# Kernel tuning notes

Measured on AMD Instinct MI355X. Metric: run time of the kernel, lower is better.

Reference implementation:

```python
import jax, jax.numpy as jnp
import numpy as np

N = 50000      # nodes
E = 800000     # edges (avg degree 16)
F_IN = 64      # node_feature_dim
D = 128        # hidden_dim == output_dim
L = 3          # num_gnn_layers
B = 8          # number of graphs in the batch
GATE_H = 128   # GraphAttentionPool hidden_dim default


def _ln(x, g, b, eps=1e-5):
    m = x.mean(-1, keepdims=True)
    v = ((x - m) ** 2).mean(-1, keepdims=True)
    return (x - m) * jax.lax.rsqrt(v + eps) * g + b


def _gelu(x):
    return jax.nn.gelu(x, approximate=False)  # torch F.gelu default = exact erf


def setup_inputs() -> dict:
    key = jax.random.key(0)
    ks = jax.random.split(key, 12)
    p = lambda k, shape: (jax.random.normal(k, shape, jnp.float32) * 0.02)
    return {
        "x": jax.random.normal(ks[0], (N, F_IN), jnp.float32),
        "edge_index": jax.random.randint(ks[1], (2, E), 0, N, dtype=jnp.int32),
        "batch": jnp.sort(jax.random.randint(ks[2], (N,), 0, B, dtype=jnp.int32)),
        # input_proj: Linear + LayerNorm
        "w_in": p(ks[3], (F_IN, D)), "b_in": jnp.zeros((D,), jnp.float32),
        "ln_in_g": jnp.ones((D,), jnp.float32), "ln_in_b": jnp.zeros((D,), jnp.float32),
        # fallback GNN layers (stacked: all layers are 2D -> D)
        "gnn_w": p(ks[4], (L, 2 * D, D)), "gnn_b": jnp.zeros((L, D), jnp.float32),
        "gnn_ln_g": jnp.ones((L, D), jnp.float32), "gnn_ln_b": jnp.zeros((L, D), jnp.float32),
        # outer per-layer norms
        "norm_g": jnp.ones((L, D), jnp.float32), "norm_b": jnp.zeros((L, D), jnp.float32),
        # attention pool gate: Linear(D,128) -> tanh -> Linear(128,1)
        "gate_w1": p(ks[5], (D, GATE_H)), "gate_b1": jnp.zeros((GATE_H,), jnp.float32),
        "gate_w2": p(ks[6], (GATE_H,)), "gate_b2": jnp.zeros((), jnp.float32),
        # out_proj: Linear + LayerNorm + GELU
        "out_w": p(ks[7], (D, D)), "out_b": jnp.zeros((D,), jnp.float32),
        "out_ln_g": jnp.ones((D,), jnp.float32), "out_ln_b": jnp.zeros((D,), jnp.float32),
    }


def reference(x, edge_index, batch, w_in, b_in, ln_in_g, ln_in_b,
              gnn_w, gnn_b, gnn_ln_g, gnn_ln_b, norm_g, norm_b,
              gate_w1, gate_b1, gate_w2, gate_b2,
              out_w, out_b, out_ln_g, out_ln_b):
    src, dst = edge_index[0], edge_index[1]
    n = x.shape[0]

    # input_proj: Linear -> LayerNorm -> GELU
    h = _gelu(_ln(x @ w_in + b_in, ln_in_g, ln_in_b))

    # in-degree count (same every layer), clamped to >= 1
    deg = jax.ops.segment_sum(jnp.ones((src.shape[0],), h.dtype), dst, num_segments=n)
    deg = jnp.maximum(deg, 1.0)[:, None]  # (N, 1)

    for i in range(L):
        # mean-neighbor aggregation: gather x[src], scatter-add to dst
        agg = jax.ops.segment_sum(h[src], dst, num_segments=n) / deg  # (N, D)
        out = jnp.concatenate([h, agg], axis=-1) @ gnn_w[i] + gnn_b[i]
        h_new = _ln(_gelu(out), gnn_ln_g[i], gnn_ln_b[i])   # layer-internal norm
        h_new = _ln(h_new, norm_g[i], norm_b[i])             # outer norm
        if i < L - 1:
            h_new = _gelu(h_new) + h                         # residual (shapes match)
        h = h_new

    # attention pool (fallback path: global softmax over all nodes)
    gate_logits = jnp.tanh(h @ gate_w1 + gate_b1) @ gate_w2 + gate_b2  # (N,)
    gate = jax.nn.softmax(gate_logits, axis=0)
    pooled = jax.ops.segment_sum(h * gate[:, None], batch, num_segments=B)  # (B, D)

    spatial_embedding = _gelu(_ln(pooled @ out_w + out_b, out_ln_g, out_ln_b))
    return spatial_embedding, h, gate
```

## Files before the change

kernel.cpp:

```cpp
#include <hip/hip_runtime.h>
#include <math.h>

#define N_NODES 50000
#define N_EDGES 800000
#define F_IN 64
#define D 128
#define NLAYER 3
#define B_GRAPHS 8
#define GB 32
#define BTH 512
#define NPW2 4
#define NBLK ((N_NODES + GB - 1) / GB)
#define ECAP 48
#define AGP 136

typedef float f32x4 __attribute__((ext_vector_type(4)));
typedef short bf16x8 __attribute__((ext_vector_type(8)));

__device__ __forceinline__ float gelu_exact(float x) {
    return 0.5f * x * (1.0f + erff(x * 0.7071067811865476f));
}

__device__ __forceinline__ unsigned short f2bf(float f) {
    unsigned int u = __float_as_uint(f);
    u = (u + 0x7fffu + ((u >> 16) & 1u)) >> 16;
    return (unsigned short)u;
}
__device__ __forceinline__ float bf2f(unsigned short u) {
    return __uint_as_float((unsigned int)u << 16);
}


__global__ void fill_direct_kernel(const int* __restrict__ src, const int* __restrict__ dst,
                                   int* __restrict__ cnt, unsigned short* __restrict__ eidx_g) {
    int e = blockIdx.x * blockDim.x + threadIdx.x;
    if (e < N_EDGES) {
        int t = dst[e];
        int pos = atomicAdd(&cnt[t], 1);
        if (pos < ECAP) eidx_g[(size_t)t * ECAP + pos] = (unsigned short)src[e];
    }
}

#define WT_GNN (NLAYER * D * 2 * D)
#define WT_G1  (WT_GNN + D * D)
#define WT_ALL (WT_G1 + D * F_IN)
__global__ void wprep_kernel(const float* __restrict__ gnn_w, const float* __restrict__ gate_w1,
                             const float* __restrict__ w_in, unsigned short* __restrict__ wt,
                             float* __restrict__ pooled, int* __restrict__ cnt) {
    int idx = blockIdx.x * 256 + threadIdx.x;
    if (blockIdx.x == 0) {
        #pragma unroll
        for (int i = 0; i < 4; ++i) pooled[threadIdx.x + i * 256] = 0.f;
    }
    if (idx < N_NODES) cnt[idx] = 0;
    if (idx >= WT_ALL) return;
    if (idx < WT_GNN) {
        int l = idx / (D * 2 * D);
        int rem = idx - l * (D * 2 * D);
        int n = rem / (2 * D);
        int k = rem - n * (2 * D);
        wt[idx] = f2bf(gnn_w[(size_t)l * 2 * D * D + (size_t)k * D + n]);
    } else if (idx < WT_G1) {
        int rem = idx - WT_GNN;
        int n = rem / D;
        int k = rem - n * D;
        wt[idx] = f2bf(gate_w1[(size_t)k * D + n]);
    } else {
        int rem = idx - WT_G1;
        int n = rem / F_IN;
        int k = rem - n * F_IN;
        wt[idx] = f2bf(w_in[(size_t)k * D + n]);
    }
}


__global__ __launch_bounds__(256) void input_proj_v5(
        const float* __restrict__ x, const unsigned short* __restrict__ wti,
        const float* __restrict__ b, const float* __restrict__ gam,
        const float* __restrict__ bet, unsigned short* __restrict__ h16) {
    __shared__ float2 red[2][GB];
    int tid = threadIdx.x;
    int wave = tid >> 6, lane = tid & 63;
    int nblk0 = blockIdx.x * GB;
    int q = lane >> 4, c = lane & 15;
    int m0 = (wave >> 1) * 16;
    int n0 = (wave & 1) * 64;
    int mrow = nblk0 + m0 + c;
    int mclamp = (mrow < N_NODES) ? mrow : (N_NODES - 1);
    const float* xr = x + (size_t)mclamp * F_IN;

    f32x4 acc[4];
    #pragma unroll
    for (int t = 0; t < 4; ++t) {
        float bn = b[n0 + t * 16 + c];
        acc[t] = (f32x4){bn, bn, bn, bn};
    }
    #pragma unroll
    for (int kk = 0; kk < 2; ++kk) {
        float4 a0 = *(const float4*)&xr[kk * 32 + q * 8];
        float4 a1 = *(const float4*)&xr[kk * 32 + q * 8 + 4];
        bf16x8 av;
        av[0] = (short)f2bf(a0.x); av[1] = (short)f2bf(a0.y);
        av[2] = (short)f2bf(a0.z); av[3] = (short)f2bf(a0.w);
        av[4] = (short)f2bf(a1.x); av[5] = (short)f2bf(a1.y);
        av[6] = (short)f2bf(a1.z); av[7] = (short)f2bf(a1.w);
        #pragma unroll
        for (int t = 0; t < 4; ++t) {
            bf16x8 bv = *(const bf16x8*)&wti[(size_t)(n0 + t * 16 + c) * F_IN + kk * 32 + q * 8];
            acc[t] = __builtin_amdgcn_mfma_f32_16x16x32_bf16(av, bv, acc[t], 0, 0, 0);
        }
    }
    float s[4], sq[4];
    #pragma unroll
    for (int r = 0; r < 4; ++r) {
        s[r] = acc[0][r] + acc[1][r] + acc[2][r] + acc[3][r];
        sq[r] = acc[0][r] * acc[0][r] + acc[1][r] * acc[1][r]
              + acc[2][r] * acc[2][r] + acc[3][r] * acc[3][r];
    }
    #pragma unroll
    for (int o = 1; o <= 8; o <<= 1)
        #pragma unroll
        for (int r = 0; r < 4; ++r) { s[r] += __shfl_xor(s[r], o); sq[r] += __shfl_xor(sq[r], o); }
    if (c == 0) {
        #pragma unroll
        for (int r = 0; r < 4; ++r) red[wave & 1][m0 + q * 4 + r] = make_float2(s[r], sq[r]);
    }
    __syncthreads();
    float gv[4], bv2[4];
    #pragma unroll
    for (int t = 0; t < 4; ++t) {
        int nn = n0 + t * 16 + c;
        gv[t] = gam[nn]; bv2[t] = bet[nn];
    }
    #pragma unroll
    for (int r = 0; r < 4; ++r) {
        int m = m0 + q * 4 + r;
        int n = nblk0 + m;
        float2 p0 = red[0][m], p1 = red[1][m];
        float mean = (p0.x + p1.x) * (1.0f / D);
        float msq  = (p0.y + p1.y) * (1.0f / D);
        float istd = rsqrtf(msq - mean * mean + 1e-5f);
        if (n < N_NODES) {
            #pragma unroll
            for (int t = 0; t < 4; ++t) {
                int nn = n0 + t * 16 + c;
                float y = (acc[t][r] - mean) * istd * gv[t] + bv2[t];
                h16[(size_t)n * D + nn] = f2bf(gelu_exact(y));
            }
        }
    }
}


__device__ __forceinline__ void acc_row(float acc[8], bf16x8 v) {
    #pragma unroll
    for (int i = 0; i < 8; ++i)
        acc[i] += __uint_as_float(((unsigned int)(unsigned short)v[i]) << 16);
}

template<int DO_GATE>
__global__ __launch_bounds__(BTH, 8) void gnn_layer_v11(
        const unsigned short* __restrict__ h16_in, unsigned short* __restrict__ h16_out,
        float* __restrict__ hf_out,
        const int* __restrict__ cnt, const unsigned short* __restrict__ eidx_g,
        const unsigned short* __restrict__ wt,
        const float* __restrict__ bias,
        const float* __restrict__ ln1g, const float* __restrict__ ln1b,
        const float* __restrict__ ln2g, const float* __restrict__ ln2b,
        int residual, int write_f32,
        const unsigned short* __restrict__ wtg,
        const float* __restrict__ gb1, const float* __restrict__ gw2,
        const float* __restrict__ gb2,
        float* __restrict__ logits, float2* __restrict__ gpart) {
    __shared__ int degs[GB];
    __shared__ int eidx[GB][32];
    __shared__ unsigned short aggb[GB][AGP];
    __shared__ float2 red1[4][GB];
    __shared__ float2 red2[4][GB];
    __shared__ float redg[4][GB];
    __shared__ float lg[GB];

    int tid = threadIdx.x;
    int wave = tid >> 6, lane = tid & 63;
    int nblk0 = blockIdx.x * GB;

    if (tid < GB) {
        int n = nblk0 + tid;
        degs[tid] = (n < N_NODES) ? cnt[n] : 0;
    }
    __syncthreads();
    #pragma unroll
    for (int k2 = 0; k2 < (GB * 32) / BTH; ++k2) {
        int f = tid + k2 * BTH;
        int g = f >> 5, sl = f & 31;
        int n = nblk0 + g;
        int dc = min(degs[g], ECAP);
        int se = (dc > 0) ? min(sl, dc - 1) : 0;
        int idx = (dc > 0) ? (int)eidx_g[(size_t)n * ECAP + se] : 0;
        eidx[g][sl] = idx;
    }
    __syncthreads();

    {
        int er = lane >> 4, dg = lane & 15;
        int gbase = wave * NPW2;
        #pragma unroll
        for (int j = 0; j < NPW2; ++j) {
            int g = gbase + j;
            int deg = degs[g];
            int id8[8];
            #pragma unroll
            for (int t = 0; t < 8; ++t) id8[t] = eidx[g][er + 4 * t];
            bf16x8 v[8];
            #pragma unroll
            for (int t = 0; t < 8; ++t)
                v[t] = *(const bf16x8*)&h16_in[(size_t)id8[t] * D + dg * 8];
            float acc[8];
            #pragma unroll
            for (int i = 0; i < 8; ++i) acc[i] = 0.f;
            #pragma unroll
            for (int t = 0; t < 8; ++t)
                if (er + 4 * t < deg) acc_row(acc, v[t]);
            int dc = min(deg, ECAP);
            if (dc > 32) {
                size_t base = (size_t)(nblk0 + g) * ECAP;
                for (int ee = 32 + er; ee < dc; ee += 4) {
                    int idx = (int)eidx_g[base + ee];
                    bf16x8 vv = *(const bf16x8*)&h16_in[(size_t)idx * D + dg * 8];
                    acc_row(acc, vv);
                }
            }
            #pragma unroll
            for (int i = 0; i < 8; ++i) {
                acc[i] += __shfl_xor(acc[i], 16);
                acc[i] += __shfl_xor(acc[i], 32);
            }
            float inv = 1.0f / fmaxf((float)deg, 1.0f);
            if (er == 0) {
                bf16x8 o;
                #pragma unroll
                for (int i = 0; i < 8; ++i) o[i] = (short)f2bf(acc[i] * inv);
                *(bf16x8*)&aggb[g][dg * 8] = o;
            }
        }
    }
    __syncthreads();

    int q = lane >> 4, c = lane & 15;
    int m0 = (wave >> 2) * 16;
    int n0 = (wave & 3) * 32;
    int mrow = nblk0 + m0 + c;
    int mclamp = (mrow < N_NODES) ? mrow : (N_NODES - 1);
    const unsigned short* arow = h16_in + (size_t)mclamp * D;

    f32x4 acc[2];
    #pragma unroll
    for (int t = 0; t < 2; ++t) {
        float bn = bias[n0 + t * 16 + c];
        acc[t] = (f32x4){bn, bn, bn, bn};
    }
    #pragma unroll
    for (int kk = 0; kk < 4; ++kk) {
        bf16x8 av = *(const bf16x8*)&arow[kk * 32 + q * 8];
        #pragma unroll
        for (int t = 0; t < 2; ++t) {
            bf16x8 bv = *(const bf16x8*)&wt[(size_t)(n0 + t * 16 + c) * 256 + kk * 32 + q * 8];
            acc[t] = __builtin_amdgcn_mfma_f32_16x16x32_bf16(av, bv, acc[t], 0, 0, 0);
        }
    }
    #pragma unroll
    for (int kk = 0; kk < 4; ++kk) {
        bf16x8 av = *(const bf16x8*)&aggb[m0 + c][kk * 32 + q * 8];
        #pragma unroll
        for (int t = 0; t < 2; ++t) {
            bf16x8 bv = *(const bf16x8*)&wt[(size_t)(n0 + t * 16 + c) * 256 + 128 + kk * 32 + q * 8];
            acc[t] = __builtin_amdgcn_mfma_f32_16x16x32_bf16(av, bv, acc[t], 0, 0, 0);
        }
    }

    float xv[2][4];
    #pragma unroll
    for (int t = 0; t < 2; ++t)
        #pragma unroll
        for (int r = 0; r < 4; ++r) xv[t][r] = gelu_exact(acc[t][r]);

    float s[4], sq[4];
    #pragma unroll
    for (int r = 0; r < 4; ++r) {
        s[r] = xv[0][r] + xv[1][r];
        sq[r] = xv[0][r] * xv[0][r] + xv[1][r] * xv[1][r];
    }
    #pragma unroll
    for (int o = 1; o <= 8; o <<= 1)
        #pragma unroll
        for (int r = 0; r < 4; ++r) { s[r] += __shfl_xor(s[r], o); sq[r] += __shfl_xor(sq[r], o); }
    int nh = wave & 3;
    if (c == 0) {
        #pragma unroll
        for (int r = 0; r < 4; ++r) red1[nh][m0 + q * 4 + r] = make_float2(s[r], sq[r]);
    }
    __syncthreads();

    float g1v[2], b1v[2], g2v[2], b2v[2];
    #pragma unroll
    for (int t = 0; t < 2; ++t) {
        int nn = n0 + t * 16 + c;
        g1v[t] = ln1g[nn]; b1v[t] = ln1b[nn];
        g2v[t] = ln2g[nn]; b2v[t] = ln2b[nn];
    }

    float y1[2][4];
    #pragma unroll
    for (int r = 0; r < 4; ++r) {
        int m = m0 + q * 4 + r;
        float2 p0 = red1[0][m], p1 = red1[1][m], p2 = red1[2][m], p3 = red1[3][m];
        float mean = (p0.x + p1.x + p2.x + p3.x) * (1.0f / D);
        float msq  = (p0.y + p1.y + p2.y + p3.y) * (1.0f / D);
        float istd = rsqrtf(msq - mean * mean + 1e-5f);
        #pragma unroll
        for (int t = 0; t < 2; ++t)
            y1[t][r] = (xv[t][r] - mean) * istd * g1v[t] + b1v[t];
    }

    #pragma unroll
    for (int r = 0; r < 4; ++r) {
        s[r] = y1[0][r] + y1[1][r];
        sq[r] = y1[0][r] * y1[0][r] + y1[1][r] * y1[1][r];
    }
    #pragma unroll
    for (int o = 1; o <= 8; o <<= 1)
        #pragma unroll
        for (int r = 0; r < 4; ++r) { s[r] += __shfl_xor(s[r], o); sq[r] += __shfl_xor(sq[r], o); }
    if (c == 0) {
        #pragma unroll
        for (int r = 0; r < 4; ++r) red2[nh][m0 + q * 4 + r] = make_float2(s[r], sq[r]);
    }
    __syncthreads();

    #pragma unroll
    for (int r = 0; r < 4; ++r) {
        int m = m0 + q * 4 + r;
        int n = nblk0 + m;
        float2 p0 = red2[0][m], p1 = red2[1][m], p2 = red2[2][m], p3 = red2[3][m];
        float mean = (p0.x + p1.x + p2.x + p3.x) * (1.0f / D);
        float msq  = (p0.y + p1.y + p2.y + p3.y) * (1.0f / D);
        float istd = rsqrtf(msq - mean * mean + 1e-5f);
        #pragma unroll
        for (int t = 0; t < 2; ++t) {
            int nn = n0 + t * 16 + c;
            float y2 = (y1[t][r] - mean) * istd * g2v[t] + b2v[t];
            float o = residual ? (gelu_exact(y2) + bf2f(h16_in[(size_t)n * D + nn])) : y2;
            if (n < N_NODES) {
                h16_out[(size_t)n * D + nn] = f2bf(o);
                if (write_f32) hf_out[(size_t)n * D + nn] = o;
            }
            if (DO_GATE) aggb[m][nn] = f2bf(o);
        }
    }

    if (DO_GATE) {
        __syncthreads();
        f32x4 gacc[2];
        #pragma unroll
        for (int t = 0; t < 2; ++t) {
            float bn = gb1[n0 + t * 16 + c];
            gacc[t] = (f32x4){bn, bn, bn, bn};
        }
        #pragma unroll
        for (int kk = 0; kk < 4; ++kk) {
            bf16x8 av = *(const bf16x8*)&aggb[m0 + c][kk * 32 + q * 8];
            #pragma unroll
            for (int t = 0; t < 2; ++t) {
                bf16x8 bv = *(const bf16x8*)&wtg[(size_t)(n0 + t * 16 + c) * 128 + kk * 32 + q * 8];
                gacc[t] = __builtin_amdgcn_mfma_f32_16x16x32_bf16(av, bv, gacc[t], 0, 0, 0);
            }
        }
        float w2v[2];
        #pragma unroll
        for (int t = 0; t < 2; ++t) w2v[t] = gw2[n0 + t * 16 + c];
        float gs[4];
        #pragma unroll
        for (int r = 0; r < 4; ++r)
            gs[r] = tanhf(gacc[0][r]) * w2v[0] + tanhf(gacc[1][r]) * w2v[1];
        #pragma unroll
        for (int o = 1; o <= 8; o <<= 1)
            #pragma unroll
            for (int r = 0; r < 4; ++r) gs[r] += __shfl_xor(gs[r], o);
        if (c == 0) {
            #pragma unroll
            for (int r = 0; r < 4; ++r) redg[nh][m0 + q * 4 + r] = gs[r];
        }
        __syncthreads();
        if ((wave & 3) == 0 && c == 0) {
            float bb2 = gb2[0];
            #pragma unroll
            for (int r = 0; r < 4; ++r) {
                int m = m0 + q * 4 + r;
                int n = nblk0 + m;
                float L = redg[0][m] + redg[1][m] + redg[2][m] + redg[3][m] + bb2;
                if (n < N_NODES) { logits[n] = L; lg[m] = L; }
                else lg[m] = -INFINITY;
            }
        }
        __syncthreads();
        if (wave == 0) {
            float l = (lane < GB) ? lg[lane] : -INFINITY;
            float mx = l;
            #pragma unroll
            for (int o = 32; o >= 1; o >>= 1) mx = fmaxf(mx, __shfl_xor(mx, o));
            float ex = (lane < GB && l > -INFINITY) ? expf(l - mx) : 0.f;
            #pragma unroll
            for (int o = 32; o >= 1; o >>= 1) ex += __shfl_xor(ex, o);
            if (lane == 0) gpart[blockIdx.x] = make_float2(mx, ex);
        }
    }
}


#define POOL_CHUNK 128
__global__ __launch_bounds__(POOL_CHUNK) void gate_pool_v2(
        const unsigned short* __restrict__ h16, const float* __restrict__ logits,
        const float2* __restrict__ gpart, const int* __restrict__ batch,
        float* __restrict__ gate_out, float* __restrict__ pooled) {
    __shared__ float sb[4];
    __shared__ float gs[POOL_CHUNK];
    __shared__ int bs[POOL_CHUNK];
    int d = threadIdx.x;
    int lane = d & 63, wv = d >> 6;
    float mx = -INFINITY;
    for (int i = d; i < NBLK; i += POOL_CHUNK) mx = fmaxf(mx, gpart[i].x);
    #pragma unroll
    for (int o = 32; o >= 1; o >>= 1) mx = fmaxf(mx, __shfl_xor(mx, o));
    if (lane == 0) sb[wv] = mx;
    __syncthreads();
    mx = fmaxf(sb[0], sb[1]);
    float ssum = 0.f;
    for (int i = d; i < NBLK; i += POOL_CHUNK) {
        float2 p = gpart[i];
        ssum += p.y * expf(p.x - mx);
    }
    #pragma unroll
    for (int o = 32; o >= 1; o >>= 1) ssum += __shfl_xor(ssum, o);
    if (lane == 0) sb[2 + wv] = ssum;
    __syncthreads();
    float inv = 1.0f / (sb[2] + sb[3]);

    int n0 = blockIdx.x * POOL_CHUNK;
    int nj = n0 + d;
    if (nj < N_NODES) {
        float gv = expf(logits[nj] - mx) * inv;
        gs[d] = gv;
        bs[d] = batch[nj];
        gate_out[nj] = gv;
    }
    __syncthreads();
    int count = min(POOL_CHUNK, N_NODES - n0);
    float acc = 0.f;
    int cur = bs[0];
    int t = 0;
    for (; t + 3 < count; t += 4) {
        float h0 = bf2f(h16[(size_t)(n0 + t + 0) * D + d]);
        float h1 = bf2f(h16[(size_t)(n0 + t + 1) * D + d]);
        float h2 = bf2f(h16[(size_t)(n0 + t + 2) * D + d]);
        float h3 = bf2f(h16[(size_t)(n0 + t + 3) * D + d]);
        int b0 = bs[t], b1 = bs[t + 1], b2 = bs[t + 2], b3 = bs[t + 3];
        if (b0 != cur) { atomicAdd(&pooled[cur * D + d], acc); acc = 0.f; cur = b0; }
        acc = fmaf(h0, gs[t], acc);
        if (b1 != cur) { atomicAdd(&pooled[cur * D + d], acc); acc = 0.f; cur = b1; }
        acc = fmaf(h1, gs[t + 1], acc);
        if (b2 != cur) { atomicAdd(&pooled[cur * D + d], acc); acc = 0.f; cur = b2; }
        acc = fmaf(h2, gs[t + 2], acc);
        if (b3 != cur) { atomicAdd(&pooled[cur * D + d], acc); acc = 0.f; cur = b3; }
        acc = fmaf(h3, gs[t + 3], acc);
    }
    for (; t < count; ++t) {
        int bn = bs[t];
        if (bn != cur) { atomicAdd(&pooled[cur * D + d], acc); acc = 0.f; cur = bn; }
        acc = fmaf(bf2f(h16[(size_t)(n0 + t) * D + d]), gs[t], acc);
    }
    atomicAdd(&pooled[cur * D + d], acc);
}

__global__ void out_proj_kernel(const float* __restrict__ pooled, const float* __restrict__ w,
                                const float* __restrict__ b, const float* __restrict__ g,
                                const float* __restrict__ beta, float* __restrict__ emb) {
    __shared__ float ps[D];
    __shared__ float sbuf[2];
    int bg = blockIdx.x, d = threadIdx.x;
    ps[d] = pooled[bg * D + d];
    __syncthreads();
    float acc = b[d];
    #pragma unroll 8
    for (int k = 0; k < D; ++k) acc += ps[k] * w[k * D + d];
    float s = acc, q = acc * acc;
    #pragma unroll
    for (int o = 32; o >= 1; o >>= 1) { s += __shfl_down(s, o); q += __shfl_down(q, o); }
    if ((d & 63) == 0) { sbuf[d >> 6] = s; }
    __syncthreads();
    float fullsum = sbuf[0] + sbuf[1];
    __syncthreads();
    if ((d & 63) == 0) { sbuf[d >> 6] = q; }
    __syncthreads();
    float fullsq = sbuf[0] + sbuf[1];
    float m = fullsum * (1.0f / D);
    float var = fullsq * (1.0f / D) - m * m;
    float y = (acc - m) * rsqrtf(var + 1e-5f) * g[d] + beta[d];
    emb[bg * D + d] = gelu_exact(y);
}

extern "C" void kernel_launch(void* const* d_in, const int* in_sizes, int n_in,
                              void* d_out, int out_size, void* d_ws, size_t ws_size,
                              hipStream_t stream) {
    const float* x        = (const float*)d_in[0];
    const int*   edge     = (const int*)d_in[1];
    const int*   batch    = (const int*)d_in[2];
    const float* w_in     = (const float*)d_in[3];
    const float* b_in     = (const float*)d_in[4];
    const float* ln_in_g  = (const float*)d_in[5];
    const float* ln_in_b  = (const float*)d_in[6];
    const float* gnn_w    = (const float*)d_in[7];
    const float* gnn_b    = (const float*)d_in[8];
    const float* gnn_ln_g = (const float*)d_in[9];
    const float* gnn_ln_b = (const float*)d_in[10];
    const float* norm_g   = (const float*)d_in[11];
    const float* norm_b   = (const float*)d_in[12];
    const float* gate_w1  = (const float*)d_in[13];
    const float* gate_b1  = (const float*)d_in[14];
    const float* gate_w2  = (const float*)d_in[15];
    const float* gate_b2  = (const float*)d_in[16];
    const float* out_w    = (const float*)d_in[17];
    const float* out_b    = (const float*)d_in[18];
    const float* out_ln_g = (const float*)d_in[19];
    const float* out_ln_b = (const float*)d_in[20];

    const int* src = edge;
    const int* dst = edge + N_EDGES;

    float* out      = (float*)d_out;
    float* emb      = out;
    float* hA       = out + B_GRAPHS * D;
    float* gate_out = hA + (size_t)N_NODES * D;

    unsigned short* h16A   = (unsigned short*)d_ws;
    unsigned short* h16B   = h16A + (size_t)N_NODES * D;
    int*            cnt    = (int*)(h16B + (size_t)N_NODES * D);
    unsigned short* eidx_g = (unsigned short*)(cnt + N_NODES);
    float*          logits = (float*)(eidx_g + (size_t)N_NODES * ECAP);
    float*          pooled = logits + N_NODES;
    float2*         gpart  = (float2*)(((uintptr_t)(pooled + B_GRAPHS * D) + 15) & ~(uintptr_t)15);
    unsigned short* wt     = (unsigned short*)(gpart + NBLK);
    unsigned short* wtg    = wt + WT_GNN;
    unsigned short* wti    = wt + WT_G1;

    wprep_kernel<<<(WT_ALL + 255) / 256, 256, 0, stream>>>(gnn_w, gate_w1, w_in, wt, pooled, cnt);
    fill_direct_kernel<<<(N_EDGES + 255) / 256, 256, 0, stream>>>(src, dst, cnt, eidx_g);

    input_proj_v5<<<NBLK, 256, 0, stream>>>(x, wti, b_in, ln_in_g, ln_in_b, h16B);

    gnn_layer_v11<0><<<NBLK, BTH, 0, stream>>>(
        h16B, h16A, hA, cnt, eidx_g, wt, gnn_b,
        gnn_ln_g, gnn_ln_b, norm_g, norm_b, 1, 0,
        nullptr, nullptr, nullptr, nullptr, nullptr, nullptr);
    gnn_layer_v11<0><<<NBLK, BTH, 0, stream>>>(
        h16A, h16B, hA, cnt, eidx_g, wt + (size_t)1 * D * 2 * D, gnn_b + D,
        gnn_ln_g + D, gnn_ln_b + D, norm_g + D, norm_b + D, 1, 0,
        nullptr, nullptr, nullptr, nullptr, nullptr, nullptr);
    gnn_layer_v11<1><<<NBLK, BTH, 0, stream>>>(
        h16B, h16A, hA, cnt, eidx_g, wt + (size_t)2 * D * 2 * D, gnn_b + 2 * D,
        gnn_ln_g + 2 * D, gnn_ln_b + 2 * D, norm_g + 2 * D, norm_b + 2 * D, 0, 1,
        wtg, gate_b1, gate_w2, gate_b2, logits, gpart);

    gate_pool_v2<<<(N_NODES + POOL_CHUNK - 1) / POOL_CHUNK, POOL_CHUNK, 0, stream>>>(
        h16A, logits, gpart, batch, gate_out, pooled);
    out_proj_kernel<<<B_GRAPHS, D, 0, stream>>>(pooled, out_w, out_b, out_ln_g, out_ln_b, emb);
}
```

Baseline: 410.9 us.

## Fuse edge fill with input proj, stage outputs via LDS, fold out_proj into pool

Merges the edge-bucketing fill into the input-projection launch as extra blocks, and folds the out_proj step into the gate-pool kernel, where the last block to finish (found with an atomic counter) runs it. Both the input projection and the GNN layer epilogues now stage results in a shared-memory buffer, so each thread writes 16-byte vectorised rows and does the residual read the same way, instead of scattered 2-byte stores. The goals are fewer kernel launches and better-coalesced global writes. The cost is extra LDS per block, which may lower occupancy in the GNN layer, plus a serial tail in the last pool block.

After: 432.0 us. 1.05x slower.

```diff
diff --git a/kernel.cpp b/kernel.cpp
--- a/kernel.cpp
+++ b/kernel.cpp
@@ -13,6 +13,8 @@
 #define NBLK ((N_NODES + GB - 1) / GB)
 #define ECAP 48
 #define AGP 136
+#define OBP 132
+#define FILL_BLKS ((N_EDGES + 255) / 256)
 
 typedef float f32x4 __attribute__((ext_vector_type(4)));
 typedef short bf16x8 __attribute__((ext_vector_type(8)));
@@ -28,17 +30,6 @@
 }
 __device__ __forceinline__ float bf2f(unsigned short u) {
     return __uint_as_float((unsigned int)u << 16);
-}
-
-
-__global__ void fill_direct_kernel(const int* __restrict__ src, const int* __restrict__ dst,
-                                   int* __restrict__ cnt, unsigned short* __restrict__ eidx_g) {
-    int e = blockIdx.x * blockDim.x + threadIdx.x;
-    if (e < N_EDGES) {
-        int t = dst[e];
-        int pos = atomicAdd(&cnt[t], 1);
-        if (pos < ECAP) eidx_g[(size_t)t * ECAP + pos] = (unsigned short)src[e];
-    }
 }
 
 #define WT_GNN (NLAYER * D * 2 * D)
@@ -46,11 +37,13 @@
 #define WT_ALL (WT_G1 + D * F_IN)
 __global__ void wprep_kernel(const float* __restrict__ gnn_w, const float* __restrict__ gate_w1,
                              const float* __restrict__ w_in, unsigned short* __restrict__ wt,
-                             float* __restrict__ pooled, int* __restrict__ cnt) {
+                             float* __restrict__ pooled, int* __restrict__ cnt,
+                             int* __restrict__ done) {
     int idx = blockIdx.x * 256 + threadIdx.x;
     if (blockIdx.x == 0) {
         #pragma unroll
         for (int i = 0; i < 4; ++i) pooled[threadIdx.x + i * 256] = 0.f;
+        if (threadIdx.x == 0) *done = 0;
     }
     if (idx < N_NODES) cnt[idx] = 0;
     if (idx >= WT_ALL) return;
@@ -74,14 +67,29 @@
 }
 
 
-__global__ __launch_bounds__(256) void input_proj_v5(
+__global__ __launch_bounds__(256) void fill_iproj_kernel(
+        const int* __restrict__ src, const int* __restrict__ dst,
+        int* __restrict__ cnt, unsigned short* __restrict__ eidx_g,
         const float* __restrict__ x, const unsigned short* __restrict__ wti,
         const float* __restrict__ b, const float* __restrict__ gam,
         const float* __restrict__ bet, unsigned short* __restrict__ h16) {
     __shared__ float2 red[2][GB];
+    __shared__ float obuf[GB][OBP];
+
+    if (blockIdx.x < FILL_BLKS) {
+        int e = blockIdx.x * 256 + threadIdx.x;
+        if (e < N_EDGES) {
+            int t = dst[e];
+            int pos = atomicAdd(&cnt[t], 1);
+            if (pos < ECAP) eidx_g[(size_t)t * ECAP + pos] = (unsigned short)src[e];
+        }
+        return;
+    }
+    int bid = blockIdx.x - FILL_BLKS;
+
     int tid = threadIdx.x;
     int wave = tid >> 6, lane = tid & 63;
-    int nblk0 = blockIdx.x * GB;
+    int nblk0 = bid * GB;
     int q = lane >> 4, c = lane & 15;
     int m0 = (wave >> 1) * 16;
     int n0 = (wave & 1) * 64;
@@ -135,17 +143,32 @@
     #pragma unroll
     for (int r = 0; r < 4; ++r) {
         int m = m0 + q * 4 + r;
-        int n = nblk0 + m;
         float2 p0 = red[0][m], p1 = red[1][m];
         float mean = (p0.x + p1.x) * (1.0f / D);
         float msq  = (p0.y + p1.y) * (1.0f / D);
         float istd = rsqrtf(msq - mean * mean + 1e-5f);
+        #pragma unroll
+        for (int t = 0; t < 4; ++t) {
+            int nn = n0 + t * 16 + c;
+            float y = (acc[t][r] - mean) * istd * gv[t] + bv2[t];
+            obuf[m][nn] = gelu_exact(y);
+        }
+    }
+    __syncthreads();
+    {
+        int row = tid >> 3, seg = tid & 7;
+        int n = nblk0 + row;
         if (n < N_NODES) {
             #pragma unroll
-            for (int t = 0; t < 4; ++t) {
-                int nn = n0 + t * 16 + c;
-                float y = (acc[t][r] - mean) * istd * gv[t] + bv2[t];
-                h16[(size_t)n * D + nn] = f2bf(gelu_exact(y));
+            for (int half = 0; half < 2; ++half) {
+                float4 f0 = *(const float4*)&obuf[row][seg * 16 + half * 8];
+                float4 f1 = *(const float4*)&obuf[row][seg * 16 + half * 8 + 4];
+                bf16x8 ov;
+                ov[0] = (short)f2bf(f0.x); ov[1] = (short)f2bf(f0.y);
+                ov[2] = (short)f2bf(f0.z); ov[3] = (short)f2bf(f0.w);
+                ov[4] = (short)f2bf(f1.x); ov[5] = (short)f2bf(f1.y);
+                ov[6] = (short)f2bf(f1.z); ov[7] = (short)f2bf(f1.w);
+                *(bf16x8*)&h16[(size_t)n * D + seg * 16 + half * 8] = ov;
             }
         }
     }
@@ -159,7 +182,7 @@
 }
 
 template<int DO_GATE>
-__global__ __launch_bounds__(BTH, 8) void gnn_layer_v11(
+__global__ __launch_bounds__(BTH, 8) void gnn_layer_v12(
         const unsigned short* __restrict__ h16_in, unsigned short* __restrict__ h16_out,
         float* __restrict__ hf_out,
         const int* __restrict__ cnt, const unsigned short* __restrict__ eidx_g,
@@ -175,6 +198,7 @@
     __shared__ int degs[GB];
     __shared__ int eidx[GB][32];
     __shared__ unsigned short aggb[GB][AGP];
+    __shared__ float obuf[GB][OBP];
     __shared__ float2 red1[4][GB];
     __shared__ float2 red2[4][GB];
     __shared__ float redg[4][GB];
@@ -340,7 +364,6 @@
     #pragma unroll
     for (int r = 0; r < 4; ++r) {
         int m = m0 + q * 4 + r;
-        int n = nblk0 + m;
         float2 p0 = red2[0][m], p1 = red2[1][m], p2 = red2[2][m], p3 = red2[3][m];
         float mean = (p0.x + p1.x + p2.x + p3.x) * (1.0f / D);
         float msq  = (p0.y + p1.y + p2.y + p3.y) * (1.0f / D);
@@ -349,13 +372,34 @@
         for (int t = 0; t < 2; ++t) {
             int nn = n0 + t * 16 + c;
             float y2 = (y1[t][r] - mean) * istd * g2v[t] + b2v[t];
-            float o = residual ? (gelu_exact(y2) + bf2f(h16_in[(size_t)n * D + nn])) : y2;
-            if (n < N_NODES) {
-                h16_out[(size_t)n * D + nn] = f2bf(o);
-                if (write_f32) hf_out[(size_t)n * D + nn] = o;
+            obuf[m][nn] = residual ? gelu_exact(y2) : y2;
+        }
+    }
+    __syncthreads();
+
+    {
+        int row = tid >> 4, seg = tid & 15;
+        int n = nblk0 + row;
+        int nclamp = (n < N_NODES) ? n : (N_NODES - 1);
+        float4 f0 = *(const float4*)&obuf[row][seg * 8];
+        float4 f1 = *(const float4*)&obuf[row][seg * 8 + 4];
+        float ov[8] = {f0.x, f0.y, f0.z, f0.w, f1.x, f1.y, f1.z, f1.w};
+        if (residual) {
+            bf16x8 hv = *(const bf16x8*)&h16_in[(size_t)nclamp * D + seg * 8];
+            #pragma unroll
+            for (int i = 0; i < 8; ++i) ov[i] += bf2f((unsigned short)hv[i]);
+        }
+        bf16x8 obv;
+        #pragma unroll
+        for (int i = 0; i < 8; ++i) obv[i] = (short)f2bf(ov[i]);
+        if (n < N_NODES) {
+            *(bf16x8*)&h16_out[(size_t)n * D + seg * 8] = obv;
+            if (write_f32) {
+                *(float4*)&hf_out[(size_t)n * D + seg * 8]     = (float4){ov[0], ov[1], ov[2], ov[3]};
+                *(float4*)&hf_out[(size_t)n * D + seg * 8 + 4] = (float4){ov[4], ov[5], ov[6], ov[7]};
             }
-            if (DO_GATE) aggb[m][nn] = f2bf(o);
-        }
+        }
+        if (DO_GATE) *(bf16x8*)&aggb[row][seg * 8] = obv;
     }
 
     if (DO_GATE) {
@@ -418,13 +462,19 @@
 
 
 #define POOL_CHUNK 128
-__global__ __launch_bounds__(POOL_CHUNK) void gate_pool_v2(
+#define POOL_BLKS ((N_NODES + POOL_CHUNK - 1) / POOL_CHUNK)
+__global__ __launch_bounds__(POOL_CHUNK) void gate_pool_v3(
         const unsigned short* __restrict__ h16, const float* __restrict__ logits,
         const float2* __restrict__ gpart, const int* __restrict__ batch,
-        float* __restrict__ gate_out, float* __restrict__ pooled) {
+        float* __restrict__ gate_out, float* __restrict__ pooled,
+        int* __restrict__ done,
+        const float* __restrict__ ow, const float* __restrict__ ob,
+        const float* __restrict__ og, const float* __restrict__ obeta,
+        float* __restrict__ emb) {
     __shared__ float sb[4];
     __shared__ float gs[POOL_CHUNK];
     __shared__ int bs[POOL_CHUNK];
+    __shared__ int amlast;
     int d = threadIdx.x;
     int lane = d & 63, wv = d >> 6;
     float mx = -INFINITY;
@@ -479,33 +529,35 @@
         acc = fmaf(bf2f(h16[(size_t)(n0 + t) * D + d]), gs[t], acc);
     }
     atomicAdd(&pooled[cur * D + d], acc);
-}
-
-__global__ void out_proj_kernel(const float* __restrict__ pooled, const float* __restrict__ w,
-                                const float* __restrict__ b, const float* __restrict__ g,
-                                const float* __restrict__ beta, float* __restrict__ emb) {
-    __shared__ float ps[D];
-    __shared__ float sbuf[2];
-    int bg = blockIdx.x, d = threadIdx.x;
-    ps[d] = pooled[bg * D + d];
-    __syncthreads();
-    float acc = b[d];
-    #pragma unroll 8
-    for (int k = 0; k < D; ++k) acc += ps[k] * w[k * D + d];
-    float s = acc, q = acc * acc;
-    #pragma unroll
-    for (int o = 32; o >= 1; o >>= 1) { s += __shfl_down(s, o); q += __shfl_down(q, o); }
-    if ((d & 63) == 0) { sbuf[d >> 6] = s; }
-    __syncthreads();
-    float fullsum = sbuf[0] + sbuf[1];
-    __syncthreads();
-    if ((d & 63) == 0) { sbuf[d >> 6] = q; }
-    __syncthreads();
-    float fullsq = sbuf[0] + sbuf[1];
-    float m = fullsum * (1.0f / D);
-    float var = fullsq * (1.0f / D) - m * m;
-    float y = (acc - m) * rsqrtf(var + 1e-5f) * g[d] + beta[d];
-    emb[bg * D + d] = gelu_exact(y);
+
+    __threadfence();
+    if (d == 0) amlast = (atomicAdd(done, 1) == POOL_BLKS - 1) ? 1 : 0;
+    __syncthreads();
+    if (!amlast) return;
+
+    for (int bg = 0; bg < B_GRAPHS; ++bg) {
+        float pk = atomicAdd(&pooled[bg * D + d], 0.0f);
+        gs[d] = pk;
+        __syncthreads();
+        float acc2 = ob[d];
+        #pragma unroll 8
+        for (int k = 0; k < D; ++k) acc2 += gs[k] * ow[(size_t)k * D + d];
+        float s2 = acc2, q2 = acc2 * acc2;
+        #pragma unroll
+        for (int o = 32; o >= 1; o >>= 1) { s2 += __shfl_down(s2, o); q2 += __shfl_down(q2, o); }
+        if (lane == 0) sb[wv] = s2;
+        __syncthreads();
+        float fullsum = sb[0] + sb[1];
+        __syncthreads();
+        if (lane == 0) sb[wv] = q2;
+        __syncthreads();
+        float fullsq = sb[0] + sb[1];
+        float m2 = fullsum * (1.0f / D);
+        float var = fullsq * (1.0f / D) - m2 * m2;
+        float y = (acc2 - m2) * rsqrtf(var + 1e-5f) * og[d] + obeta[d];
+        emb[bg * D + d] = gelu_exact(y);
+        __syncthreads();
+    }
 }
 
 extern "C" void kernel_launch(void* const* d_in, const int* in_sizes, int n_in,
@@ -547,30 +599,31 @@
     unsigned short* eidx_g = (unsigned short*)(cnt + N_NODES);
     float*          logits = (float*)(eidx_g + (size_t)N_NODES * ECAP);
     float*          pooled = logits + N_NODES;
-    float2*         gpart  = (float2*)(((uintptr_t)(pooled + B_GRAPHS * D) + 15) & ~(uintptr_t)15);
+    int*            done   = (int*)(pooled + B_GRAPHS * D);
+    float2*         gpart  = (float2*)(((uintptr_t)(done + 4) + 15) & ~(uintptr_t)15);
     unsigned short* wt     = (unsigned short*)(gpart + NBLK);
     unsigned short* wtg    = wt + WT_GNN;
     unsigned short* wti    = wt + WT_G1;
 
-    wprep_kernel<<<(WT_ALL + 255) / 256, 256, 0, stream>>>(gnn_w, gate_w1, w_in, wt, pooled, cnt);
-    fill_direct_kernel<<<(N_EDGES + 255) / 256, 256, 0, stream>>>(src, dst, cnt, eidx_g);
-
-    input_proj_v5<<<NBLK, 256, 0, stream>>>(x, wti, b_in, ln_in_g, ln_in_b, h16B);
-
-    gnn_layer_v11<0><<<NBLK, BTH, 0, stream>>>(
+    wprep_kernel<<<(WT_ALL + 255) / 256, 256, 0, stream>>>(
+        gnn_w, gate_w1, w_in, wt, pooled, cnt, done);
+    fill_iproj_kernel<<<FILL_BLKS + NBLK, 256, 0, stream>>>(
+        src, dst, cnt, eidx_g, x, wti, b_in, ln_in_g, ln_in_b, h16B);
+
+    gnn_layer_v12<0><<<NBLK, BTH, 0, stream>>>(
         h16B, h16A, hA, cnt, eidx_g, wt, gnn_b,
         gnn_ln_g, gnn_ln_b, norm_g, norm_b, 1, 0,
         nullptr, nullptr, nullptr, nullptr, nullptr, nullptr);
-    gnn_layer_v11<0><<<NBLK, BTH, 0, stream>>>(
+    gnn_layer_v12<0><<<NBLK, BTH, 0, stream>>>(
         h16A, h16B, hA, cnt, eidx_g, wt + (size_t)1 * D * 2 * D, gnn_b + D,
         gnn_ln_g + D, gnn_ln_b + D, norm_g + D, norm_b + D, 1, 0,
         nullptr, nullptr, nullptr, nullptr, nullptr, nullptr);
-    gnn_layer_v11<1><<<NBLK, BTH, 0, stream>>>(
+    gnn_layer_v12<1><<<NBLK, BTH, 0, stream>>>(
         h16B, h16A, hA, cnt, eidx_g, wt + (size_t)2 * D * 2 * D, gnn_b + 2 * D,
         gnn_ln_g + 2 * D, gnn_ln_b + 2 * D, norm_g + 2 * D, norm_b + 2 * D, 0, 1,
         wtg, gate_b1, gate_w2, gate_b2, logits, gpart);
 
-    gate_pool_v2<<<(N_NODES + POOL_CHUNK - 1) / POOL_CHUNK, POOL_CHUNK, 0, stream>>>(
-        h16A, logits, gpart, batch, gate_out, pooled);
-    out_proj_kernel<<<B_GRAPHS, D, 0, stream>>>(pooled, out_w, out_b, out_ln_g, out_ln_b, emb);
-}
+    gate_pool_v3<<<POOL_BLKS, POOL_CHUNK, 0, stream>>>(
+        h16A, logits, gpart, batch, gate_out, pooled, done,
+        out_w, out_b, out_ln_g, out_ln_b, emb);
+}
```

## Gather neighbor features from an FP8 copy and stage outputs through shared memory

Applied to the files above, without the earlier changes.

Each layer and the input projection now also write an FP8 (e4m3) copy of the node features. The neighbor aggregation gathers these 8-byte rows instead of 16-byte bf16 rows, halving the random-gather traffic that dominates each layer. Epilogue outputs are staged in an LDS float buffer so bf16, fp8 and fp32 stores become wide, coalesced vector writes. The cost is extra write traffic for the FP8 copy, more shared memory per block that may lower occupancy, and noticeably lower precision in the mean aggregation.

After: 398.7 us. 1.03x faster.

```diff
diff --git a/kernel.cpp b/kernel.cpp
--- a/kernel.cpp
+++ b/kernel.cpp
@@ -13,6 +13,7 @@
 #define NBLK ((N_NODES + GB - 1) / GB)
 #define ECAP 48
 #define AGP 136
+#define OBP 132
 
 typedef float f32x4 __attribute__((ext_vector_type(4)));
 typedef short bf16x8 __attribute__((ext_vector_type(8)));
@@ -28,6 +29,13 @@
 }
 __device__ __forceinline__ float bf2f(unsigned short u) {
     return __uint_as_float((unsigned int)u << 16);
+}
+
+__device__ __forceinline__ unsigned int pk_fp8_lo(float a, float b, unsigned int old) {
+    return (unsigned int)__builtin_amdgcn_cvt_pk_fp8_f32(a, b, (int)old, false);
+}
+__device__ __forceinline__ unsigned int pk_fp8_hi(float a, float b, unsigned int old) {
+    return (unsigned int)__builtin_amdgcn_cvt_pk_fp8_f32(a, b, (int)old, true);
 }
 
 
@@ -74,11 +82,13 @@
 }
 
 
-__global__ __launch_bounds__(256) void input_proj_v5(
+__global__ __launch_bounds__(256) void input_proj_v6(
         const float* __restrict__ x, const unsigned short* __restrict__ wti,
         const float* __restrict__ b, const float* __restrict__ gam,
-        const float* __restrict__ bet, unsigned short* __restrict__ h16) {
+        const float* __restrict__ bet, unsigned short* __restrict__ h16,
+        unsigned char* __restrict__ h8) {
     __shared__ float2 red[2][GB];
+    __shared__ float obuf[GB][OBP];
     int tid = threadIdx.x;
     int wave = tid >> 6, lane = tid & 63;
     int nblk0 = blockIdx.x * GB;
@@ -135,32 +145,56 @@
     #pragma unroll
     for (int r = 0; r < 4; ++r) {
         int m = m0 + q * 4 + r;
-        int n = nblk0 + m;
         float2 p0 = red[0][m], p1 = red[1][m];
         float mean = (p0.x + p1.x) * (1.0f / D);
         float msq  = (p0.y + p1.y) * (1.0f / D);
         float istd = rsqrtf(msq - mean * mean + 1e-5f);
+        #pragma unroll
+        for (int t = 0; t < 4; ++t) {
+            int nn = n0 + t * 16 + c;
+            float y = (acc[t][r] - mean) * istd * gv[t] + bv2[t];
+            obuf[m][nn] = gelu_exact(y);
+        }
+    }
+    __syncthreads();
+    {
+        int row = tid >> 3, seg = tid & 7;
+        int n = nblk0 + row;
         if (n < N_NODES) {
             #pragma unroll
-            for (int t = 0; t < 4; ++t) {
-                int nn = n0 + t * 16 + c;
-                float y = (acc[t][r] - mean) * istd * gv[t] + bv2[t];
-                h16[(size_t)n * D + nn] = f2bf(gelu_exact(y));
-            }
-        }
-    }
-}
-
-
-__device__ __forceinline__ void acc_row(float acc[8], bf16x8 v) {
-    #pragma unroll
-    for (int i = 0; i < 8; ++i)
-        acc[i] += __uint_as_float(((unsigned int)(unsigned short)v[i]) << 16);
+            for (int half = 0; half < 2; ++half) {
+                float4 f0 = *(const float4*)&obuf[row][seg * 16 + half * 8];
+                float4 f1 = *(const float4*)&obuf[row][seg * 16 + half * 8 + 4];
+                bf16x8 ov;
+                ov[0] = (short)f2bf(f0.x); ov[1] = (short)f2bf(f0.y);
+                ov[2] = (short)f2bf(f0.z); ov[3] = (short)f2bf(f0.w);
+                ov[4] = (short)f2bf(f1.x); ov[5] = (short)f2bf(f1.y);
+                ov[6] = (short)f2bf(f1.z); ov[7] = (short)f2bf(f1.w);
+                *(bf16x8*)&h16[(size_t)n * D + seg * 16 + half * 8] = ov;
+                unsigned int lo = pk_fp8_lo(f0.x, f0.y, 0u);
+                lo = pk_fp8_hi(f0.z, f0.w, lo);
+                unsigned int hi = pk_fp8_lo(f1.x, f1.y, 0u);
+                hi = pk_fp8_hi(f1.z, f1.w, hi);
+                *(uint2*)&h8[(size_t)n * D + seg * 16 + half * 8] = make_uint2(lo, hi);
+            }
+        }
+    }
+}
+
+
+__device__ __forceinline__ void acc_row8(float acc[8], uint2 w) {
+    auto a0 = __builtin_amdgcn_cvt_pk_f32_fp8((int)w.x, false);
+    auto a1 = __builtin_amdgcn_cvt_pk_f32_fp8((int)w.x, true);
+    auto a2 = __builtin_amdgcn_cvt_pk_f32_fp8((int)w.y, false);
+    auto a3 = __builtin_amdgcn_cvt_pk_f32_fp8((int)w.y, true);
+    acc[0] += a0[0]; acc[1] += a0[1]; acc[2] += a1[0]; acc[3] += a1[1];
+    acc[4] += a2[0]; acc[5] += a2[1]; acc[6] += a3[0]; acc[7] += a3[1];
 }
 
 template<int DO_GATE>
-__global__ __launch_bounds__(BTH, 8) void gnn_layer_v11(
-        const unsigned short* __restrict__ h16_in, unsigned short* __restrict__ h16_out,
+__global__ __launch_bounds__(BTH, 8) void gnn_layer_v13(
+        const unsigned short* __restrict__ h16_in, const unsigned char* __restrict__ h8_in,
+        unsigned short* __restrict__ h16_out, unsigned char* __restrict__ h8_out,
         float* __restrict__ hf_out,
         const int* __restrict__ cnt, const unsigned short* __restrict__ eidx_g,
         const unsigned short* __restrict__ wt,
@@ -175,6 +209,7 @@
     __shared__ int degs[GB];
     __shared__ int eidx[GB][32];
     __shared__ unsigned short aggb[GB][AGP];
+    __shared__ float obuf[GB][OBP];
     __shared__ float2 red1[4][GB];
     __shared__ float2 red2[4][GB];
     __shared__ float redg[4][GB];
@@ -211,23 +246,23 @@
             int id8[8];
             #pragma unroll
             for (int t = 0; t < 8; ++t) id8[t] = eidx[g][er + 4 * t];
-            bf16x8 v[8];
+            uint2 v[8];
             #pragma unroll
             for (int t = 0; t < 8; ++t)
-                v[t] = *(const bf16x8*)&h16_in[(size_t)id8[t] * D + dg * 8];
+                v[t] = *(const uint2*)&h8_in[(size_t)id8[t] * D + dg * 8];
             float acc[8];
             #pragma unroll
             for (int i = 0; i < 8; ++i) acc[i] = 0.f;
             #pragma unroll
             for (int t = 0; t < 8; ++t)
-                if (er + 4 * t < deg) acc_row(acc, v[t]);
+                if (er + 4 * t < deg) acc_row8(acc, v[t]);
             int dc = min(deg, ECAP);
             if (dc > 32) {
                 size_t base = (size_t)(nblk0 + g) * ECAP;
                 for (int ee = 32 + er; ee < dc; ee += 4) {
                     int idx = (int)eidx_g[base + ee];
-                    bf16x8 vv = *(const bf16x8*)&h16_in[(size_t)idx * D + dg * 8];
-                    acc_row(acc, vv);
+                    uint2 vv = *(const uint2*)&h8_in[(size_t)idx * D + dg * 8];
+                    acc_row8(acc, vv);
                 }
             }
             #pragma unroll
@@ -340,7 +375,6 @@
     #pragma unroll
     for (int r = 0; r < 4; ++r) {
         int m = m0 + q * 4 + r;
-        int n = nblk0 + m;
         float2 p0 = red2[0][m], p1 = red2[1][m], p2 = red2[2][m], p3 = red2[3][m];
         float mean = (p0.x + p1.x + p2.x + p3.x) * (1.0f / D);
         float msq  = (p0.y + p1.y + p2.y + p3.y) * (1.0f / D);
@@ -349,13 +383,41 @@
         for (int t = 0; t < 2; ++t) {
             int nn = n0 + t * 16 + c;
             float y2 = (y1[t][r] - mean) * istd * g2v[t] + b2v[t];
-            float o = residual ? (gelu_exact(y2) + bf2f(h16_in[(size_t)n * D + nn])) : y2;
-            if (n < N_NODES) {
-                h16_out[(size_t)n * D + nn] = f2bf(o);
-                if (write_f32) hf_out[(size_t)n * D + nn] = o;
-            }
-            if (DO_GATE) aggb[m][nn] = f2bf(o);
-        }
+            obuf[m][nn] = residual ? gelu_exact(y2) : y2;
+        }
+    }
+    __syncthreads();
+
+    {
+        int row = tid >> 4, seg = tid & 15;
+        int n = nblk0 + row;
+        int nclamp = (n < N_NODES) ? n : (N_NODES - 1);
+        float4 f0 = *(const float4*)&obuf[row][seg * 8];
+        float4 f1 = *(const float4*)&obuf[row][seg * 8 + 4];
+        float ov[8] = {f0.x, f0.y, f0.z, f0.w, f1.x, f1.y, f1.z, f1.w};
+        if (residual) {
+            bf16x8 hv = *(const bf16x8*)&h16_in[(size_t)nclamp * D + seg * 8];
+            #pragma unroll
+            for (int i = 0; i < 8; ++i) ov[i] += bf2f((unsigned short)hv[i]);
+        }
+        bf16x8 obv;
+        #pragma unroll
+        for (int i = 0; i < 8; ++i) obv[i] = (short)f2bf(ov[i]);
+        if (n < N_NODES) {
+            *(bf16x8*)&h16_out[(size_t)n * D + seg * 8] = obv;
+            if (h8_out) {
+                unsigned int lo = pk_fp8_lo(ov[0], ov[1], 0u);
+                lo = pk_fp8_hi(ov[2], ov[3], lo);
+                unsigned int hi = pk_fp8_lo(ov[4], ov[5], 0u);
+                hi = pk_fp8_hi(ov[6], ov[7], hi);
+                *(uint2*)&h8_out[(size_t)n * D + seg * 8] = make_uint2(lo, hi);
+            }
+            if (write_f32) {
+                *(float4*)&hf_out[(size_t)n * D + seg * 8]     = (float4){ov[0], ov[1], ov[2], ov[3]};
+                *(float4*)&hf_out[(size_t)n * D + seg * 8 + 4] = (float4){ov[4], ov[5], ov[6], ov[7]};
+            }
+        }
+        if (DO_GATE) *(bf16x8*)&aggb[row][seg * 8] = obv;
     }
 
     if (DO_GATE) {
@@ -543,7 +605,9 @@
 
     unsigned short* h16A   = (unsigned short*)d_ws;
     unsigned short* h16B   = h16A + (size_t)N_NODES * D;
-    int*            cnt    = (int*)(h16B + (size_t)N_NODES * D);
+    unsigned char*  h8A    = (unsigned char*)(h16B + (size_t)N_NODES * D);
+    unsigned char*  h8B    = h8A + (size_t)N_NODES * D;
+    int*            cnt    = (int*)(h8B + (size_t)N_NODES * D);
     unsigned short* eidx_g = (unsigned short*)(cnt + N_NODES);
     float*          logits = (float*)(eidx_g + (size_t)N_NODES * ECAP);
     float*          pooled = logits + N_NODES;
@@ -555,18 +619,18 @@
     wprep_kernel<<<(WT_ALL + 255) / 256, 256, 0, stream>>>(gnn_w, gate_w1, w_in, wt, pooled, cnt);
     fill_direct_kernel<<<(N_EDGES + 255) / 256, 256, 0, stream>>>(src, dst, cnt, eidx_g);
 
-    input_proj_v5<<<NBLK, 256, 0, stream>>>(x, wti, b_in, ln_in_g, ln_in_b, h16B);
-
-    gnn_layer_v11<0><<<NBLK, BTH, 0, stream>>>(
-        h16B, h16A, hA, cnt, eidx_g, wt, gnn_b,
+    input_proj_v6<<<NBLK, 256, 0, stream>>>(x, wti, b_in, ln_in_g, ln_in_b, h16B, h8B);
+
+    gnn_layer_v13<0><<<NBLK, BTH, 0, stream>>>(
+        h16B, h8B, h16A, h8A, hA, cnt, eidx_g, wt, gnn_b,
         gnn_ln_g, gnn_ln_b, norm_g, norm_b, 1, 0,
         nullptr, nullptr, nullptr, nullptr, nullptr, nullptr);
-    gnn_layer_v11<0><<<NBLK, BTH, 0, stream>>>(
-        h16A, h16B, hA, cnt, eidx_g, wt + (size_t)1 * D * 2 * D, gnn_b + D,
+    gnn_layer_v13<0><<<NBLK, BTH, 0, stream>>>(
+        h16A, h8A, h16B, h8B, hA, cnt, eidx_g, wt + (size_t)1 * D * 2 * D, gnn_b + D,
         gnn_ln_g + D, gnn_ln_b + D, norm_g + D, norm_b + D, 1, 0,
         nullptr, nullptr, nullptr, nullptr, nullptr, nullptr);
-    gnn_layer_v11<1><<<NBLK, BTH, 0, stream>>>(
-        h16B, h16A, hA, cnt, eidx_g, wt + (size_t)2 * D * 2 * D, gnn_b + 2 * D,
+    gnn_layer_v13<1><<<NBLK, BTH, 0, stream>>>(
+        h16B, h8B, h16A, nullptr, hA, cnt, eidx_g, wt + (size_t)2 * D * 2 * D, gnn_b + 2 * D,
         gnn_ln_g + 2 * D, gnn_ln_b + 2 * D, norm_g + 2 * D, norm_b + 2 * D, 0, 1,
         wtg, gate_b1, gate_w2, gate_b2, logits, gpart);
 
```
